# Kernel optimization log

Measured on AMD Instinct MI355X. Metric: run time of the kernel, lower is better.

The kernel has to match this reference:

```python
import jax, jax.numpy as jnp
import numpy as np


def _position_table(seq_len, d_model, dtype):
    # position[i, j] = sin(i / 10000**((j+1)/d))  if j even
    #                  cos(i / 10000**((j+1)/d))  if j odd
    # (note the nonstandard (j+1)/d exponent, faithful to the source)
    i = jnp.arange(seq_len, dtype=dtype)[:, None]          # [S, 1]
    j = jnp.arange(d_model, dtype=dtype)[None, :]          # [1, D]
    pf = i / jnp.power(jnp.asarray(10000.0, dtype), (j + 1.0) / d_model)  # [S, D]
    even = (jnp.arange(d_model) % 2 == 0)[None, :]
    return jnp.where(even, jnp.sin(pf), jnp.cos(pf))       # [S, D]


def setup_inputs() -> dict:
    key = jax.random.key(0)
    x = jax.random.normal(key, (4, 8192, 1024), dtype=jnp.float32)
    return {"x": x}


def reference(x) -> jnp.ndarray:
    B, S, D = x.shape
    pos = _position_table(S, D, x.dtype)
    return x + pos[None, :, :]
```

## Files before the change

kernel.cpp:

```cpp
#include <hip/hip_runtime.h>
#include <math.h>

#define PE_S 8192
#define PE_D 1024
#define PE_B 4

#define PE_K 8
#define PE_QTOTAL (PE_B * PE_S * PE_D / 4)
#define PE_NT (PE_QTOTAL / PE_K)
#define PE_THREADS 256
#define PE_BLOCKS (PE_NT / PE_THREADS)

typedef float f32x4 __attribute__((ext_vector_type(4)));

__device__ __forceinline__ float pe_sin(float fs, float wrev) {
    float t = fs * wrev;
    float r = t - floorf(t);
    r += fmaf(fs, wrev, -t);
    return __builtin_amdgcn_sinf(r);
}
__device__ __forceinline__ float pe_cos(float fs, float wrev) {
    float t = fs * wrev;
    float r = t - floorf(t);
    r += fmaf(fs, wrev, -t);
    return __builtin_amdgcn_cosf(r);
}

__global__ __launch_bounds__(PE_THREADS) void position_encoder_kernel(
    const float* __restrict__ x, float* __restrict__ out) {
    const int tid = blockIdx.x * blockDim.x + threadIdx.x;
    const int d0  = (tid & (PE_D / 4 - 1)) << 2;

    const float A2 = -0.012976281620653760f;
    const float C  = -2.6514961294723187f;
    const float w0 = exp2f(fmaf((float)(d0 + 1), A2, C));
    const float w1 = exp2f(fmaf((float)(d0 + 2), A2, C));
    const float w2 = exp2f(fmaf((float)(d0 + 3), A2, C));
    const float w3 = exp2f(fmaf((float)(d0 + 4), A2, C));

    f32x4 v[PE_K];
#pragma unroll
    for (int k = 0; k < PE_K; ++k) {
        v[k] = *reinterpret_cast<const f32x4*>(
            x + (size_t)(tid + k * PE_NT) * 4);
    }

    __builtin_amdgcn_sched_barrier(0);

#pragma unroll
    for (int k = 0; k < PE_K; ++k) {
        const int q = tid + k * PE_NT;
        const int s = (q >> 8) & (PE_S - 1);
        const float fs = (float)s;

        f32x4 p;
        p.x = pe_sin(fs, w0);
        p.y = pe_cos(fs, w1);
        p.z = pe_sin(fs, w2);
        p.w = pe_cos(fs, w3);

        *reinterpret_cast<f32x4*>(out + (size_t)q * 4) = v[k] + p;
    }
}

extern "C" void kernel_launch(void* const* d_in, const int* in_sizes, int n_in,
                              void* d_out, int out_size, void* d_ws, size_t ws_size,
                              hipStream_t stream) {
    const float* x = (const float*)d_in[0];
    float* out = (float*)d_out;
    position_encoder_kernel<<<PE_BLOCKS, PE_THREADS, 0, stream>>>(x, out);
}
```

Before: 241.6 us.

## Load input directly to LDS and overlap with sin/cos compute

Replaces the register-destined vector loads of x with global_load_lds transfers into a per-wave shared-memory buffer. The positional sin/cos values are computed while those loads are in flight, then the kernel waits on vmcnt, reads back from LDS and stores the sum. This aims to free the registers that held the loaded values and to hide the transcendental work under memory latency, at the cost of an extra LDS round trip and 32KB of LDS per block, which may limit occupancy.

```diff
diff --git a/kernel.cpp b/kernel.cpp
--- a/kernel.cpp
+++ b/kernel.cpp
@@ -6,9 +6,9 @@
 #define PE_B 4
 
 #define PE_K 8
+#define PE_THREADS 256
 #define PE_QTOTAL (PE_B * PE_S * PE_D / 4)
 #define PE_NT (PE_QTOTAL / PE_K)
-#define PE_THREADS 256
 #define PE_BLOCKS (PE_NT / PE_THREADS)
 
 typedef float f32x4 __attribute__((ext_vector_type(4)));
@@ -28,8 +28,24 @@
 
 __global__ __launch_bounds__(PE_THREADS) void position_encoder_kernel(
     const float* __restrict__ x, float* __restrict__ out) {
+    __shared__ __attribute__((aligned(16)))
+        float lds[(PE_THREADS / 64) * PE_K * 256];
+
     const int tid = blockIdx.x * blockDim.x + threadIdx.x;
+    const int wv  = threadIdx.x >> 6;
+    const int ln  = threadIdx.x & 63;
     const int d0  = (tid & (PE_D / 4 - 1)) << 2;
+
+    float* lbase = &lds[wv * (PE_K * 256)];
+
+#pragma unroll
+    for (int k = 0; k < PE_K; ++k) {
+        const size_t goff = (size_t)(tid + k * PE_NT) * 4;
+        __builtin_amdgcn_global_load_lds(
+            (const __attribute__((address_space(1))) void*)(x + goff),
+            (__attribute__((address_space(3))) void*)(lbase + k * 256),
+            16, 0, 0);
+    }
 
     const float A2 = -0.012976281620653760f;
     const float C  = -2.6514961294723187f;
@@ -38,28 +54,26 @@
     const float w2 = exp2f(fmaf((float)(d0 + 3), A2, C));
     const float w3 = exp2f(fmaf((float)(d0 + 4), A2, C));
 
-    f32x4 v[PE_K];
+    f32x4 p[PE_K];
 #pragma unroll
     for (int k = 0; k < PE_K; ++k) {
-        v[k] = *reinterpret_cast<const f32x4*>(
-            x + (size_t)(tid + k * PE_NT) * 4);
+        const int q = tid + k * PE_NT;
+        const float fs = (float)((q >> 8) & (PE_S - 1));
+        p[k].x = pe_sin(fs, w0);
+        p[k].y = pe_cos(fs, w1);
+        p[k].z = pe_sin(fs, w2);
+        p[k].w = pe_cos(fs, w3);
     }
 
+    __builtin_amdgcn_sched_barrier(0);
+    __builtin_amdgcn_s_waitcnt(0x0f70);
     __builtin_amdgcn_sched_barrier(0);
 
 #pragma unroll
     for (int k = 0; k < PE_K; ++k) {
-        const int q = tid + k * PE_NT;
-        const int s = (q >> 8) & (PE_S - 1);
-        const float fs = (float)s;
-
-        f32x4 p;
-        p.x = pe_sin(fs, w0);
-        p.y = pe_cos(fs, w1);
-        p.z = pe_sin(fs, w2);
-        p.w = pe_cos(fs, w3);
-
-        *reinterpret_cast<f32x4*>(out + (size_t)q * 4) = v[k] + p;
+        const size_t q = (size_t)tid + (size_t)k * PE_NT;
+        const f32x4 v = *reinterpret_cast<const f32x4*>(&lbase[k * 256 + ln * 4]);
+        *reinterpret_cast<f32x4*>(out + q * 4) = v + p[k];
     }
 }
 
```

New measurement: 242.3 us. Within noise of the previous version (+0.3%).
